# Optimization experiments

Measured on AMD Instinct MI355X. Metric: run time of the kernel, lower is better.

## Reference

```python
import jax, jax.numpy as jnp
import numpy as np

C = 512
CQ = C // 8
BN_EPS = 1e-5


def setup_inputs() -> dict:
    key = jax.random.key(0)
    ks = jax.random.split(key, 12)
    s = 0.02
    return {
        "x": jax.random.normal(ks[0], (4, C, 64, 64), dtype=jnp.float32),
        "qw": jax.random.normal(ks[1], (CQ, C), dtype=jnp.float32) * s,
        "qb": jnp.zeros((CQ,), dtype=jnp.float32),
        "kw": jax.random.normal(ks[2], (CQ, C), dtype=jnp.float32) * s,
        "kb": jnp.zeros((CQ,), dtype=jnp.float32),
        "vw": jax.random.normal(ks[3], (C, C), dtype=jnp.float32) * s,
        "vb": jnp.zeros((C,), dtype=jnp.float32),
        "gamma": jnp.zeros((1,), dtype=jnp.float32),
        "beta": jnp.zeros((1,), dtype=jnp.float32),
        "fw": jax.random.normal(ks[4], (C, 2 * C), dtype=jnp.float32) * s,
        "fb": jnp.zeros((C,), dtype=jnp.float32),
        "bn_w": jnp.ones((C,), dtype=jnp.float32),
        "bn_b": jnp.zeros((C,), dtype=jnp.float32),
    }


def reference(x, qw, qb, kw, kb, vw, vb, gamma, beta, fw, fb, bn_w, bn_b):
    b, c, h, w = x.shape
    n = h * w
    xf = x.reshape(b, c, n)  # [b, c, n]

    # ----- position attention -----
    q = jnp.einsum('oc,bcn->bon', qw, xf) + qb[None, :, None]  # [b, cq, n]
    k = jnp.einsum('oc,bcn->bon', kw, xf) + kb[None, :, None]
    v = jnp.einsum('oc,bcn->bon', vw, xf) + vb[None, :, None]  # [b, c, n]
    # scores[i, j] = q_i . k_j, softmax over j
    scores = jnp.einsum('bci,bcj->bij', q, k)  # [b, n, n]
    att = jax.nn.softmax(scores, axis=-1)
    pos = jnp.einsum('bcj,bij->bci', v, att)  # [b, c, n]
    pos_out = (gamma[0] * pos + xf).reshape(b, c, h, w)

    # ----- channel attention -----
    energy = jnp.einsum('bin,bjn->bij', xf, xf)  # [b, c, c]
    catt = jax.nn.softmax(energy, axis=-1)
    chan = jnp.einsum('bij,bjn->bin', catt, xf)
    chan_out = (beta[0] * chan + xf).reshape(b, c, h, w)

    # ----- fusion: 1x1 conv + BN (batch stats, training mode) + ReLU -----
    cat = jnp.concatenate([pos_out, chan_out], axis=1)  # [b, 2c, h, w]
    y = jnp.einsum('oc,bchw->bohw', fw, cat) + fb[None, :, None, None]
    mean = jnp.mean(y, axis=(0, 2, 3), keepdims=True)
    var = jnp.var(y, axis=(0, 2, 3), keepdims=True)
    yn = (y - mean) * jax.lax.rsqrt(var + BN_EPS)
    out = jax.nn.relu(yn * bn_w[None, :, None, None] + bn_b[None, :, None, None])
    return out
```

## Files before the change

kernel.cpp:

```cpp
#include <hip/hip_runtime.h>
#include <stdint.h>

typedef unsigned short u16;
typedef __attribute__((ext_vector_type(8))) short bf16x8;
typedef __attribute__((ext_vector_type(4))) float f32x4;

#define DEVI static __device__ __forceinline__

DEVI u16 f2bf(float f){
  union { float f; uint32_t u; } c; c.f = f;
  uint32_t u = c.u;
  u += 0x7FFFu + ((u >> 16) & 1u);
  return (u16)(u >> 16);
}
DEVI float b2f(u16 h){
  union { uint32_t u; float f; } c; c.u = ((uint32_t)h) << 16;
  return c.f;
}

DEVI void gload16(const u16* g, u16* l){
  __builtin_amdgcn_global_load_lds(
      (const __attribute__((address_space(1))) unsigned int*)g,
      (__attribute__((address_space(3))) unsigned int*)l, 16, 0, 0);
}

DEVI bf16x8 ldsrd(const void* base, int byte){
  return *reinterpret_cast<const bf16x8*>((const char*)base + byte);
}

template<int BM,int BN,int FM,int FN,int BIAS,int EPI,int SWZ,int KSPLIT=1>
__global__ __launch_bounds__(256) void gemm_bt(
    const u16* __restrict__ A, long long strideA, int lda,
    const u16* __restrict__ B, long long strideB, int ldb,
    void* __restrict__ C, long long strideC, int ldc,
    const float* __restrict__ bias, int K,
    const float* __restrict__ cscale, const u16* __restrict__ xadd,
    long long strideX, int ldx, float* __restrict__ red)
{
  constexpr int BK  = 32;
  constexpr int WTM = FM*16, WTN = FN*16;
  static_assert(BM == 2*WTM && BN == 2*WTN, "2x2 wave layout");
  __shared__ u16 As[BM*BK];
  __shared__ u16 Bs[BN*BK];

  int bx = blockIdx.x, by = blockIdx.y, bz = blockIdx.z;
  if(SWZ){
    const int gx = gridDim.x, gy = gridDim.y;
    const int nwg = gx * gy * gridDim.z;
    const int orig = bx + gx * (by + gy * bz);
    const int q = nwg >> 3, r = nwg & 7;
    const int xcd = orig & 7, i = orig >> 3;
    const int wg = (xcd < r ? xcd*(q+1) : r*(q+1) + (xcd-r)*q) + i;
    bx = wg % gx;
    const int t = wg / gx;
    by = t % gy;
    bz = t / gy;
  }

  const int zz = bz;
  const int z  = (KSPLIT > 1) ? zz / KSPLIT : zz;
  const int ks = (KSPLIT > 1) ? zz % KSPLIT : 0;
  const u16* Ab = A + (long long)z * strideA + (long long)ks * K;
  const u16* Bb = B + (long long)z * strideB + (long long)ks * K;

  const int tid  = threadIdx.x;
  const int lane = tid & 63, wid = tid >> 6;
  const int wr = wid >> 1, wc = wid & 1;
  const long long bm0 = (long long)by * BM;
  const long long bn0 = (long long)bx * BN;

  const int srow  = lane >> 2;
  const int scol  = (((lane & 3) ^ ((lane >> 3) & 3))) * 8;
  const int wrow  = wid * 16 + srow;
  constexpr int TA = BM/64, TB = BN/64;

  const int fr  = lane & 15;
  const int sl8 = ((lane >> 4) ^ ((lane >> 1) & 3)) * 8;

  f32x4 acc[FM][FN] = {};

  for(int k0 = 0; k0 < K; k0 += BK){
    __syncthreads();
    #pragma unroll
    for(int t=0;t<TA;t++)
      gload16(&Ab[(bm0 + t*64 + wrow)*lda + k0 + scol],
              &As[(t*64 + wid*16)*BK]);
    #pragma unroll
    for(int t=0;t<TB;t++)
      gload16(&Bb[(bn0 + t*64 + wrow)*ldb + k0 + scol],
              &Bs[(t*64 + wid*16)*BK]);
    __syncthreads();

    bf16x8 af[FM], bg[FN];
    #pragma unroll
    for(int m=0;m<FM;m++)
      af[m] = *reinterpret_cast<const bf16x8*>(&As[(wr*WTM + m*16 + fr)*BK + sl8]);
    #pragma unroll
    for(int n=0;n<FN;n++)
      bg[n] = *reinterpret_cast<const bf16x8*>(&Bs[(wc*WTN + n*16 + fr)*BK + sl8]);
    #pragma unroll
    for(int m=0;m<FM;m++)
      #pragma unroll
      for(int n=0;n<FN;n++)
        acc[m][n] = __builtin_amdgcn_mfma_f32_16x16x32_bf16(af[m], bg[n], acc[m][n], 0, 0, 0);
  }

  const int lr = (lane >> 4) * 4, lc = lane & 15;

  if(EPI == 8){
    u16* Cp = (u16*)C + (long long)zz*strideC;
    #pragma unroll
    for(int n=0;n<FN;n++){
      long long col = bn0 + wc*WTN + n*16 + lc;
      float bv = bias[(int)col];
      float s = 0.f, ss = 0.f;
      #pragma unroll
      for(int m=0;m<FM;m++){
        #pragma unroll
        for(int r=0;r<4;r++){
          long long row = bm0 + wr*WTM + m*16 + lr + r;
          long long idx = row*(long long)ldc + col;
          float v = acc[m][n][r] + bv + b2f(Cp[idx]);
          Cp[idx] = f2bf(v);
          s += v; ss += v*v;
        }
      }
      s += __shfl_xor(s,16); ss += __shfl_xor(ss,16);
      s += __shfl_xor(s,32); ss += __shfl_xor(ss,32);
      if(lane < 16){
        int slot = (z*(int)gridDim.y + by)*2 + wr;
        red[col*512 + slot*2]     = s;
        red[col*512 + slot*2 + 1] = ss;
      }
    }
    return;
  }

  const float g = (EPI == 3) ? cscale[0] : 0.f;
  #pragma unroll
  for(int m=0;m<FM;m++){
    #pragma unroll
    for(int n=0;n<FN;n++){
      #pragma unroll
      for(int r=0;r<4;r++){
        long long row = bm0 + wr*WTM + m*16 + lr + r;
        long long col = bn0 + wc*WTN + n*16 + lc;
        float v = acc[m][n][r];
        if(BIAS == 1) v += bias[(int)row];
        if(BIAS == 2) v += bias[(int)col];
        long long idx = row * (long long)ldc + col;
        if(EPI == 0){
          ((float*)C + (long long)zz*strideC)[idx] = v;
        } else if(EPI == 1){
          ((float*)C + (long long)zz*strideC)[idx] += v;
        } else if(EPI == 2){
          ((u16*)C + (long long)zz*strideC)[idx] = f2bf(v);
        } else {
          float xv = b2f(xadd[(long long)z*strideX + row*(long long)ldx + col]);
          ((u16*)C + (long long)zz*strideC)[idx] = f2bf(g * v + xv);
        }
      }
    }
  }
}

__global__ __launch_bounds__(512, 4) void flash_pos(
    const u16* __restrict__ qkT,
    const u16* __restrict__ vB,
    u16* __restrict__ yT,
    const float* __restrict__ gamma)
{
  __shared__ u16 Ks[2][64*64];
  __shared__ u16 Vs[256*64];
  __shared__ u16 Ps[64*64];
  __shared__ float RS[2][4][32];

  int flat = blockIdx.x + 64*(blockIdx.y + 2*blockIdx.z);
  flat = (flat & 7)*64 + (flat >> 3);
  const int bx = flat & 63;
  const int ch = (flat >> 6) & 1;
  const int z  = flat >> 7;

  const int q0 = bx*64, c0 = ch*256;
  const int tid = threadIdx.x, lane = tid & 63, wid = tid >> 6;
  const int wr = wid >> 2, wc = wid & 3;
  const int fr = lane & 15, fq = lane >> 4;

  const u16* qkb = qkT + (long long)z*4096*128;
  const u16* vbb = vB  + (long long)z*512*4096;

  const int srow  = lane >> 3;
  const int sslot = (lane & 7) ^ srow;

  bf16x8 qa[2][2];
  #pragma unroll
  for(int m=0;m<2;m++)
    #pragma unroll
    for(int kk=0;kk<2;kk++)
      qa[m][kk] = *reinterpret_cast<const bf16x8*>(
          &qkb[(long long)(q0 + wr*32 + m*16 + fr)*128 + kk*32 + fq*8]);

  const u16* kp  = qkb + (long long)(wid*8 + srow)*128 + 64 + sslot*8;
  const u16* vp0 = vbb + (long long)(c0 + wid*8 + srow)*4096 + sslot*8;

  const int xm   = (fr & 7) << 4;
  const int koff = (wc*16 + fr)*128 + ((fq*16) ^ xm);
  const int pab  = (wr*32 + fr)*128 + ((fq*16) ^ xm);
  const int vfb  = (wc*64 + fr)*128 + ((fq*16) ^ xm);
  const int kdst = wid * 1024;
  const int key2 = (wc*16 + fr)*2;
  int pwo[4];
  #pragma unroll
  for(int r=0;r<4;r++){
    int qr = fq*4 + r;
    pwo[r] = qr*128 + (key2 ^ ((qr & 7) << 4));
  }

  gload16(kp, (u16*)((char*)Ks + kdst));
  kp += 64*128;
  gload16(vp0,            &Vs[(  0 + wid*8)*64]);
  gload16(vp0 +  64*4096, &Vs[( 64 + wid*8)*64]);
  gload16(vp0 + 128*4096, &Vs[(128 + wid*8)*64]);
  gload16(vp0 + 192*4096, &Vs[(192 + wid*8)*64]);
  vp0 += 64;
  __syncthreads();

  f32x4 acc[2][4] = {};
  float rsacc[2][4] = {};

  for(int t=0;t<64;t++){
    const int kbase = (t & 1) ? 8192 : 0;
    bf16x8 kb0 = ldsrd(Ks, kbase + koff);
    bf16x8 kb1 = ldsrd(Ks, kbase + (koff ^ 64));
    f32x4 s[2] = {};
    #pragma unroll
    for(int m=0;m<2;m++){
      s[m] = __builtin_amdgcn_mfma_f32_16x16x32_bf16(qa[m][0], kb0, s[m], 0, 0, 0);
      s[m] = __builtin_amdgcn_mfma_f32_16x16x32_bf16(qa[m][1], kb1, s[m], 0, 0, 0);
    }

    #pragma unroll
    for(int m=0;m<2;m++){
      float e0 = exp2f(s[m][0]), e1 = exp2f(s[m][1]);
      float e2 = exp2f(s[m][2]), e3 = exp2f(s[m][3]);
      rsacc[m][0] += e0; rsacc[m][1] += e1;
      rsacc[m][2] += e2; rsacc[m][3] += e3;
      char* pbase = (char*)Ps + wr*4096 + m*2048;
      *(u16*)(pbase + pwo[0]) = f2bf(e0);
      *(u16*)(pbase + pwo[1]) = f2bf(e1);
      *(u16*)(pbase + pwo[2]) = f2bf(e2);
      *(u16*)(pbase + pwo[3]) = f2bf(e3);
    }
    __syncthreads();

    if(t+1 < 64){
      gload16(kp, (u16*)((char*)Ks + (kbase ^ 8192) + kdst));
      kp += 64*128;
    }

    bf16x8 pa00 = ldsrd(Ps, pab);
    bf16x8 pa01 = ldsrd(Ps, pab ^ 64);
    bf16x8 pa10 = ldsrd(Ps, (pab + 2048));
    bf16x8 pa11 = ldsrd(Ps, (pab + 2048) ^ 64);
    __builtin_amdgcn_s_setprio(1);
    #pragma unroll
    for(int n=0;n<4;n++){
      bf16x8 v0 = ldsrd(Vs, vfb + n*2048);
      bf16x8 v1 = ldsrd(Vs, (vfb + n*2048) ^ 64);
      acc[0][n] = __builtin_amdgcn_mfma_f32_16x16x32_bf16(pa00, v0, acc[0][n], 0, 0, 0);
      acc[0][n] = __builtin_amdgcn_mfma_f32_16x16x32_bf16(pa01, v1, acc[0][n], 0, 0, 0);
      acc[1][n] = __builtin_amdgcn_mfma_f32_16x16x32_bf16(pa10, v0, acc[1][n], 0, 0, 0);
      acc[1][n] = __builtin_amdgcn_mfma_f32_16x16x32_bf16(pa11, v1, acc[1][n], 0, 0, 0);
    }
    __builtin_amdgcn_s_setprio(0);
    __syncthreads();

    if(t+1 < 64){
      gload16(vp0,            &Vs[(  0 + wid*8)*64]);
      gload16(vp0 +  64*4096, &Vs[( 64 + wid*8)*64]);
      gload16(vp0 + 128*4096, &Vs[(128 + wid*8)*64]);
      gload16(vp0 + 192*4096, &Vs[(192 + wid*8)*64]);
      vp0 += 64;
    }
  }

  #pragma unroll
  for(int m=0;m<2;m++)
    #pragma unroll
    for(int r=0;r<4;r++){
      float v = rsacc[m][r];
      #pragma unroll
      for(int o=1;o<16;o<<=1) v += __shfl_xor(v, o);
      rsacc[m][r] = v;
    }
  if(fr == 0){
    #pragma unroll
    for(int m=0;m<2;m++)
      #pragma unroll
      for(int r=0;r<4;r++)
        RS[wr][wc][m*16 + fq*4 + r] = rsacc[m][r];
  }
  __syncthreads();

  const float g = gamma[0];
  u16* yb = yT + (long long)z*4096*512;
  #pragma unroll
  for(int m=0;m<2;m++){
    float inv[4];
    #pragma unroll
    for(int r=0;r<4;r++){
      int rloc = m*16 + fq*4 + r;
      inv[r] = g / (RS[wr][0][rloc] + RS[wr][1][rloc] +
                    RS[wr][2][rloc] + RS[wr][3][rloc]);
    }
    #pragma unroll
    for(int n=0;n<4;n++){
      #pragma unroll
      for(int r=0;r<4;r++){
        int qrow = q0 + wr*32 + m*16 + fq*4 + r;
        int c    = c0 + wc*64 + n*16 + fr;
        yb[(long long)qrow*512 + c] = f2bf(acc[m][n][r]*inv[r]);
      }
    }
  }
}

__global__ __launch_bounds__(256) void esum_stats(const u16* __restrict__ part,
                                                  float* __restrict__ st)
{
  const int row = blockIdx.x;
  const int b = row >> 9, i = row & 511;
  const int t = threadIdx.x;
  const int lane = t & 63, wid = t >> 6;
  float v0 = 0.f, v1 = 0.f;
  #pragma unroll
  for(int sl=0;sl<4;sl++){
    uint32_t pr = *reinterpret_cast<const uint32_t*>(
        &part[(((long long)(b*4 + sl)*512 + i)*512) + 2*t]);
    v0 += b2f((u16)pr);
    v1 += b2f((u16)(pr >> 16));
  }
  float m = fmaxf(v0, v1);
  #pragma unroll
  for(int o=32;o;o>>=1) m = fmaxf(m, __shfl_xor(m, o));
  __shared__ float sred[4];
  if(lane == 0) sred[wid] = m;
  __syncthreads();
  m = fmaxf(fmaxf(sred[0], sred[1]), fmaxf(sred[2], sred[3]));
  float s = __expf(v0 - m) + __expf(v1 - m);
  #pragma unroll
  for(int o=32;o;o>>=1) s += __shfl_xor(s, o);
  __syncthreads();
  if(lane == 0) sred[wid] = s;
  __syncthreads();
  if(t == 0){
    st[row*2]   = m;
    st[row*2+1] = sred[0] + sred[1] + sred[2] + sred[3];
  }
}

__global__ __launch_bounds__(256) void catt_apply(const u16* __restrict__ part,
                                                  const float* __restrict__ st,
                                                  u16* __restrict__ cattT)
{
  const int row = blockIdx.x;
  const int b = row >> 9, i = row & 511;
  const int t = threadIdx.x;
  float v0 = 0.f, v1 = 0.f;
  #pragma unroll
  for(int sl=0;sl<4;sl++){
    uint32_t pr = *reinterpret_cast<const uint32_t*>(
        &part[(((long long)(b*4 + sl)*512 + i)*512) + 2*t]);
    v0 += b2f((u16)pr);
    v1 += b2f((u16)(pr >> 16));
  }
  float4 ms = reinterpret_cast<const float4*>(st)[b*256 + t];
  float o0 = __expf(v0 - ms.x) / ms.y;
  float o1 = __expf(v1 - ms.z) / ms.w;
  uint32_t pk = (uint32_t)f2bf(o0) | ((uint32_t)f2bf(o1) << 16);
  *reinterpret_cast<uint32_t*>(&cattT[(long long)row * 512 + 2*t]) = pk;
}

__global__ __launch_bounds__(256) void prep_weights(
    const float* __restrict__ qw, const float* __restrict__ kw,
    const float* __restrict__ vw, const float* __restrict__ fw,
    const float* __restrict__ qb, const float* __restrict__ kb,
    u16* __restrict__ qkwb, u16* __restrict__ vwT, u16* __restrict__ fwb,
    u16* __restrict__ fw12, float* __restrict__ qkb)
{
  const float LOG2E = 1.4426950408889634f;
  long long i = (long long)blockIdx.x*256 + threadIdx.x;
  if(i < 8192){
    float4 v = reinterpret_cast<const float4*>(qw)[i];
    ushort4 w = { f2bf(v.x*LOG2E), f2bf(v.y*LOG2E), f2bf(v.z*LOG2E), f2bf(v.w*LOG2E) };
    reinterpret_cast<ushort4*>(qkwb)[i] = w;
  } else if(i < 16384){
    long long o = i - 8192;
    float4 v = reinterpret_cast<const float4*>(kw)[o];
    ushort4 w = { f2bf(v.x), f2bf(v.y), f2bf(v.z), f2bf(v.w) };
    reinterpret_cast<ushort4*>(qkwb + 32768)[o] = w;
  } else if(i < 81920){
    long long o = i - 16384;
    float4 v = reinterpret_cast<const float4*>(vw)[o];
    int c  = (int)(o >> 7);
    int cp = (int)(o & 127) * 4;
    vwT[(cp+0)*512 + c] = f2bf(v.x);
    vwT[(cp+1)*512 + c] = f2bf(v.y);
    vwT[(cp+2)*512 + c] = f2bf(v.z);
    vwT[(cp+3)*512 + c] = f2bf(v.w);
  } else if(i < 212992){
    long long o = i - 81920;
    float4 v = reinterpret_cast<const float4*>(fw)[o];
    ushort4 w = { f2bf(v.x), f2bf(v.y), f2bf(v.z), f2bf(v.w) };
    reinterpret_cast<ushort4*>(fwb)[o] = w;
    int row = (int)(o >> 8);
    int c4  = (int)(o & 255) * 4;
    if(c4 < 512){
      float4 v2 = reinterpret_cast<const float4*>(fw)[o + 128];
      ushort4 s = { f2bf(v.x+v2.x), f2bf(v.y+v2.y), f2bf(v.z+v2.z), f2bf(v.w+v2.w) };
      reinterpret_cast<ushort4*>(fw12)[row*128 + (c4>>2)] = s;
    }
  } else if(i < 213024){
    int t = (int)(i - 212992) * 4;
    #pragma unroll
    for(int j=0;j<4;j++) qkb[t+j] = (t+j < 64) ? qb[t+j]*LOG2E : kb[t+j-64];
  }
}

__global__ __launch_bounds__(256) void fwvb(const float* __restrict__ fw,
                                            const float* __restrict__ vb,
                                            float* __restrict__ bp)
{
  int o = blockIdx.x*256 + threadIdx.x;
  if(o >= 512) return;
  float s = 0.f;
  for(int c=0;c<512;c++) s += fw[o*1024 + c] * vb[c];
  bp[o] = s;
}

__global__ __launch_bounds__(256) void transpose_cast(
    const float* __restrict__ x, u16* __restrict__ xfb, u16* __restrict__ xfT)
{
  __shared__ float tile[32][33];
  const int b  = blockIdx.z;
  const int n0 = blockIdx.x * 32, c0 = blockIdx.y * 32;
  const int tx = threadIdx.x, ty = threadIdx.y;
  const float* xp = x + (long long)b * 512 * 4096;
  #pragma unroll
  for(int i=0;i<4;i++){
    int c = c0 + ty + i*8;
    float v = xp[(long long)c*4096 + n0 + tx];
    tile[ty + i*8][tx] = v;
    xfb[((long long)b*512 + c)*4096 + n0 + tx] = f2bf(v);
  }
  __syncthreads();
  #pragma unroll
  for(int i=0;i<4;i++){
    int n = n0 + ty + i*8;
    xfT[((long long)b*4096 + n)*512 + c0 + tx] = f2bf(tile[tx][ty + i*8]);
  }
}

__global__ __launch_bounds__(256) void bn_finalize(const float* __restrict__ red,
                                                   float* __restrict__ stat)
{
  int ch = blockIdx.x*256 + threadIdx.x;
  if(ch >= 512) return;
  float s = 0.f, ss = 0.f;
  for(int j=0;j<256;j++){
    s  += red[ch*512 + j*2];
    ss += red[ch*512 + j*2 + 1];
  }
  float mean = s * (1.f/16384.f);
  float var  = ss * (1.f/16384.f) - mean*mean;
  stat[ch*2]   = mean;
  stat[ch*2+1] = rsqrtf(var + 1e-5f);
}

__global__ __launch_bounds__(256) void bn_apply_t(const u16* __restrict__ yT,
    const float* __restrict__ stat, const float* __restrict__ w,
    const float* __restrict__ bb, float* __restrict__ out)
{
  __shared__ float tile[32][33];
  const int b  = blockIdx.z;
  const int n0 = blockIdx.x * 32, c0 = blockIdx.y * 32;
  const int tx = threadIdx.x, ty = threadIdx.y;
  const int ch = c0 + tx;
  const float sc = w[ch] * stat[ch*2+1];
  const float sh = bb[ch] - stat[ch*2] * sc;
  #pragma unroll
  for(int i=0;i<4;i++){
    int n = n0 + ty + i*8;
    float v = b2f(yT[((long long)b*4096 + n)*512 + ch]);
    tile[ty + i*8][tx] = fmaxf(v*sc + sh, 0.f);
  }
  __syncthreads();
  #pragma unroll
  for(int i=0;i<4;i++){
    int c = c0 + ty + i*8;
    out[((long long)b*512 + c)*4096 + n0 + tx] = tile[tx][ty + i*8];
  }
}

extern "C" void kernel_launch(void* const* d_in, const int* in_sizes, int n_in,
                              void* d_out, int out_size, void* d_ws, size_t ws_size,
                              hipStream_t stream)
{
  const float* x     = (const float*)d_in[0];
  const float* qw    = (const float*)d_in[1];
  const float* qb    = (const float*)d_in[2];
  const float* kw    = (const float*)d_in[3];
  const float* kb    = (const float*)d_in[4];
  const float* vw    = (const float*)d_in[5];
  const float* vb    = (const float*)d_in[6];
  const float* gamma = (const float*)d_in[7];
  const float* beta  = (const float*)d_in[8];
  const float* fw    = (const float*)d_in[9];
  const float* fb    = (const float*)d_in[10];
  const float* bnw   = (const float*)d_in[11];
  const float* bnb   = (const float*)d_in[12];
  float* out = (float*)d_out;
  (void)in_sizes; (void)n_in; (void)out_size; (void)ws_size;

  char* base = (char*)d_ws;
  size_t off = 0;
  auto alloc = [&](size_t bytes)->char* {
    char* p = base + off;
    off += (bytes + 255) & ~(size_t)255;
    return p;
  };
  const long long NB = 4, Cc = 512, Nn = 4096;

  u16*   xfT  = (u16*)alloc((size_t)NB*Nn*Cc*2);
  u16*   xfb  = (u16*)alloc((size_t)NB*Cc*Nn*2);
  u16*   fwb  = (u16*)alloc((size_t)Cc*2*Cc*2);
  u16*   qkwb = (u16*)alloc((size_t)128*Cc*2);
  float* qkb  = (float*)alloc(128*4);
  u16*   vwT  = (u16*)alloc((size_t)Cc*Cc*2);
  u16*   Wp   = (u16*)alloc((size_t)Cc*Cc*2);
  u16*   fw12 = (u16*)alloc((size_t)Cc*Cc*2);
  float* bp   = (float*)alloc(Cc*4);
  u16*   qkT  = (u16*)alloc((size_t)NB*Nn*128*2);
  u16*   vB   = (u16*)alloc((size_t)NB*Cc*Nn*2);
  u16*   epart= (u16*)alloc((size_t)16*Cc*Cc*2);
  u16*   cattT= (u16*)alloc((size_t)NB*Cc*Cc*2);
  u16*   Mb   = (u16*)alloc((size_t)NB*Cc*Cc*2);
  float* st2  = (float*)alloc((size_t)NB*Cc*2*4);
  float* stat = (float*)alloc((size_t)Cc*2*4);
  float* red  = (float*)alloc((size_t)Cc*256*2*4);
  u16*   yT   = xfb;

  prep_weights<<<dim3(833), dim3(256), 0, stream>>>(qw, kw, vw, fw, qb, kb,
                                                    qkwb, vwT, fwb, fw12, qkb);
  fwvb<<<dim3(2), dim3(256), 0, stream>>>(fw, vb, bp);
  transpose_cast<<<dim3(128,16,4), dim3(32,8), 0, stream>>>(x, xfb, xfT);

  gemm_bt<64,64,2,2,0,2,1><<<dim3(8,8,1), dim3(256), 0, stream>>>(
      fwb, 0, 1024, vwT, 0, 512, Wp, 0, 512, nullptr, 512,
      nullptr, nullptr, 0, 0, nullptr);

  gemm_bt<64,128,2,4,2,2,1><<<dim3(1,64,4), dim3(256), 0, stream>>>(
      xfT, Nn*Cc, 512, qkwb, 0, 512, qkT, Nn*128, 128, qkb, 512,
      nullptr, nullptr, 0, 0, nullptr);
  gemm_bt<128,128,4,4,1,2,1><<<dim3(32,4,4), dim3(256), 0, stream>>>(
      Wp, 0, 512, xfT, Nn*Cc, 512, vB, Cc*Nn, 4096, bp, 512,
      nullptr, nullptr, 0, 0, nullptr);

  gemm_bt<128,128,4,4,0,2,1,4><<<dim3(4,4,16), dim3(256), 0, stream>>>(
      xfb, Cc*Nn, 4096, xfb, Cc*Nn, 4096, epart, Cc*Cc, 512, nullptr, 1024,
      nullptr, nullptr, 0, 0, nullptr);
  esum_stats<<<dim3(2048), dim3(256), 0, stream>>>(epart, st2);
  catt_apply<<<dim3(2048), dim3(256), 0, stream>>>(epart, st2, cattT);

  gemm_bt<64,64,2,2,0,3,1><<<dim3(8,8,4), dim3(256), 0, stream>>>(
      fwb + 512, 0, 1024, cattT, Cc*Cc, 512, Mb, Cc*Cc, 512, nullptr, 512,
      beta, fw12, 0, 512, nullptr);

  flash_pos<<<dim3(64,2,4), dim3(512), 0, stream>>>(qkT, vB, yT, gamma);

  gemm_bt<128,128,4,4,2,8,1><<<dim3(4,32,4), dim3(256), 0, stream>>>(
      xfT, Nn*Cc, 512, Mb, Cc*Cc, 512, yT, Nn*Cc, 512, fb, 512,
      nullptr, nullptr, 0, 0, red);

  bn_finalize<<<dim3(2), dim3(256), 0, stream>>>(red, stat);
  bn_apply_t<<<dim3(128,16,4), dim3(32,8), 0, stream>>>(yT, stat, bnw, bnb, out);
}
```

Before: 275.8 us.

## Double flash_pos query tile to 128 rows and fold fwvb into prep_weights

The position-attention flash kernel now handles 128 queries per block instead of 64. Its 8 waves are rearranged as 4x2, so each wave computes a 32x32 score tile and a 32x128 output tile. Each K/V tile loaded into LDS is reused across twice as many queries, halving global K/V traffic and the number of blocks, at the cost of more accumulator registers (acc grows from 8 to 16 f32x4) and fewer blocks in flight (256 vs 512). The small fw·vb bias kernel is also merged into prep_weights, saving one launch.

```diff
diff --git a/kernel.cpp b/kernel.cpp
--- a/kernel.cpp
+++ b/kernel.cpp
@@ -172,18 +172,18 @@
 {
   __shared__ u16 Ks[2][64*64];
   __shared__ u16 Vs[256*64];
-  __shared__ u16 Ps[64*64];
-  __shared__ float RS[2][4][32];
-
-  int flat = blockIdx.x + 64*(blockIdx.y + 2*blockIdx.z);
-  flat = (flat & 7)*64 + (flat >> 3);
-  const int bx = flat & 63;
-  const int ch = (flat >> 6) & 1;
-  const int z  = flat >> 7;
-
-  const int q0 = bx*64, c0 = ch*256;
+  __shared__ u16 Ps[128*64];
+  __shared__ float RS[4][2][32];
+
+  int flat = blockIdx.x + 32*(blockIdx.y + 2*blockIdx.z);
+  flat = (flat & 7)*32 + (flat >> 3);
+  const int bx = flat & 31;
+  const int ch = (flat >> 5) & 1;
+  const int z  = flat >> 6;
+
+  const int q0 = bx*128, c0 = ch*256;
   const int tid = threadIdx.x, lane = tid & 63, wid = tid >> 6;
-  const int wr = wid >> 2, wc = wid & 3;
+  const int wr = wid >> 1, wc = wid & 1;
   const int fr = lane & 15, fq = lane >> 4;
 
   const u16* qkb = qkT + (long long)z*4096*128;
@@ -204,17 +204,11 @@
   const u16* vp0 = vbb + (long long)(c0 + wid*8 + srow)*4096 + sslot*8;
 
   const int xm   = (fr & 7) << 4;
-  const int koff = (wc*16 + fr)*128 + ((fq*16) ^ xm);
+  const int koff = (wc*32 + fr)*128 + ((fq*16) ^ xm);
   const int pab  = (wr*32 + fr)*128 + ((fq*16) ^ xm);
-  const int vfb  = (wc*64 + fr)*128 + ((fq*16) ^ xm);
+  const int vfb  = (wc*128 + fr)*128 + ((fq*16) ^ xm);
   const int kdst = wid * 1024;
-  const int key2 = (wc*16 + fr)*2;
-  int pwo[4];
-  #pragma unroll
-  for(int r=0;r<4;r++){
-    int qr = fq*4 + r;
-    pwo[r] = qr*128 + (key2 ^ ((qr & 7) << 4));
-  }
+  const int pkey0 = (wc*32 + fr)*2;
 
   gload16(kp, (u16*)((char*)Ks + kdst));
   kp += 64*128;
@@ -225,31 +219,40 @@
   vp0 += 64;
   __syncthreads();
 
-  f32x4 acc[2][4] = {};
+  f32x4 acc[2][8] = {};
   float rsacc[2][4] = {};
 
   for(int t=0;t<64;t++){
     const int kbase = (t & 1) ? 8192 : 0;
-    bf16x8 kb0 = ldsrd(Ks, kbase + koff);
-    bf16x8 kb1 = ldsrd(Ks, kbase + (koff ^ 64));
-    f32x4 s[2] = {};
+    bf16x8 kb[2][2];
+    #pragma unroll
+    for(int n=0;n<2;n++)
+      #pragma unroll
+      for(int kk=0;kk<2;kk++)
+        kb[n][kk] = ldsrd(Ks, kbase + ((koff + n*2048) ^ (kk*64)));
+    f32x4 s[2][2] = {};
+    #pragma unroll
+    for(int m=0;m<2;m++)
+      #pragma unroll
+      for(int n=0;n<2;n++)
+        #pragma unroll
+        for(int kk=0;kk<2;kk++)
+          s[m][n] = __builtin_amdgcn_mfma_f32_16x16x32_bf16(qa[m][kk], kb[n][kk], s[m][n], 0, 0, 0);
+
     #pragma unroll
     for(int m=0;m<2;m++){
-      s[m] = __builtin_amdgcn_mfma_f32_16x16x32_bf16(qa[m][0], kb0, s[m], 0, 0, 0);
-      s[m] = __builtin_amdgcn_mfma_f32_16x16x32_bf16(qa[m][1], kb1, s[m], 0, 0, 0);
-    }
-
-    #pragma unroll
-    for(int m=0;m<2;m++){
-      float e0 = exp2f(s[m][0]), e1 = exp2f(s[m][1]);
-      float e2 = exp2f(s[m][2]), e3 = exp2f(s[m][3]);
-      rsacc[m][0] += e0; rsacc[m][1] += e1;
-      rsacc[m][2] += e2; rsacc[m][3] += e3;
       char* pbase = (char*)Ps + wr*4096 + m*2048;
-      *(u16*)(pbase + pwo[0]) = f2bf(e0);
-      *(u16*)(pbase + pwo[1]) = f2bf(e1);
-      *(u16*)(pbase + pwo[2]) = f2bf(e2);
-      *(u16*)(pbase + pwo[3]) = f2bf(e3);
+      #pragma unroll
+      for(int n=0;n<2;n++){
+        const int pkey = pkey0 + n*32;
+        #pragma unroll
+        for(int r=0;r<4;r++){
+          float e = exp2f(s[m][n][r]);
+          rsacc[m][r] += e;
+          int qr = fq*4 + r;
+          *(u16*)(pbase + qr*128 + (pkey ^ ((qr & 7) << 4))) = f2bf(e);
+        }
+      }
     }
     __syncthreads();
 
@@ -258,19 +261,21 @@
       kp += 64*128;
     }
 
-    bf16x8 pa00 = ldsrd(Ps, pab);
-    bf16x8 pa01 = ldsrd(Ps, pab ^ 64);
-    bf16x8 pa10 = ldsrd(Ps, (pab + 2048));
-    bf16x8 pa11 = ldsrd(Ps, (pab + 2048) ^ 64);
+    bf16x8 pa[2][2];
+    #pragma unroll
+    for(int m=0;m<2;m++)
+      #pragma unroll
+      for(int kk=0;kk<2;kk++)
+        pa[m][kk] = ldsrd(Ps, (pab + m*2048) ^ (kk*64));
     __builtin_amdgcn_s_setprio(1);
     #pragma unroll
-    for(int n=0;n<4;n++){
-      bf16x8 v0 = ldsrd(Vs, vfb + n*2048);
-      bf16x8 v1 = ldsrd(Vs, (vfb + n*2048) ^ 64);
-      acc[0][n] = __builtin_amdgcn_mfma_f32_16x16x32_bf16(pa00, v0, acc[0][n], 0, 0, 0);
-      acc[0][n] = __builtin_amdgcn_mfma_f32_16x16x32_bf16(pa01, v1, acc[0][n], 0, 0, 0);
-      acc[1][n] = __builtin_amdgcn_mfma_f32_16x16x32_bf16(pa10, v0, acc[1][n], 0, 0, 0);
-      acc[1][n] = __builtin_amdgcn_mfma_f32_16x16x32_bf16(pa11, v1, acc[1][n], 0, 0, 0);
+    for(int n=0;n<8;n++){
+      #pragma unroll
+      for(int kk=0;kk<2;kk++){
+        bf16x8 v = ldsrd(Vs, (vfb + n*2048) ^ (kk*64));
+        acc[0][n] = __builtin_amdgcn_mfma_f32_16x16x32_bf16(pa[0][kk], v, acc[0][n], 0, 0, 0);
+        acc[1][n] = __builtin_amdgcn_mfma_f32_16x16x32_bf16(pa[1][kk], v, acc[1][n], 0, 0, 0);
+      }
     }
     __builtin_amdgcn_s_setprio(0);
     __syncthreads();
@@ -310,15 +315,14 @@
     #pragma unroll
     for(int r=0;r<4;r++){
       int rloc = m*16 + fq*4 + r;
-      inv[r] = g / (RS[wr][0][rloc] + RS[wr][1][rloc] +
-                    RS[wr][2][rloc] + RS[wr][3][rloc]);
-    }
-    #pragma unroll
-    for(int n=0;n<4;n++){
+      inv[r] = g / (RS[wr][0][rloc] + RS[wr][1][rloc]);
+    }
+    #pragma unroll
+    for(int n=0;n<8;n++){
       #pragma unroll
       for(int r=0;r<4;r++){
         int qrow = q0 + wr*32 + m*16 + fq*4 + r;
-        int c    = c0 + wc*64 + n*16 + fr;
+        int c    = c0 + wc*128 + n*16 + fr;
         yb[(long long)qrow*512 + c] = f2bf(acc[m][n][r]*inv[r]);
       }
     }
@@ -385,8 +389,9 @@
     const float* __restrict__ qw, const float* __restrict__ kw,
     const float* __restrict__ vw, const float* __restrict__ fw,
     const float* __restrict__ qb, const float* __restrict__ kb,
+    const float* __restrict__ vb,
     u16* __restrict__ qkwb, u16* __restrict__ vwT, u16* __restrict__ fwb,
-    u16* __restrict__ fw12, float* __restrict__ qkb)
+    u16* __restrict__ fw12, float* __restrict__ qkb, float* __restrict__ bp)
 {
   const float LOG2E = 1.4426950408889634f;
   long long i = (long long)blockIdx.x*256 + threadIdx.x;
@@ -424,18 +429,12 @@
     int t = (int)(i - 212992) * 4;
     #pragma unroll
     for(int j=0;j<4;j++) qkb[t+j] = (t+j < 64) ? qb[t+j]*LOG2E : kb[t+j-64];
-  }
-}
-
-__global__ __launch_bounds__(256) void fwvb(const float* __restrict__ fw,
-                                            const float* __restrict__ vb,
-                                            float* __restrict__ bp)
-{
-  int o = blockIdx.x*256 + threadIdx.x;
-  if(o >= 512) return;
-  float s = 0.f;
-  for(int c=0;c<512;c++) s += fw[o*1024 + c] * vb[c];
-  bp[o] = s;
+  } else if(i < 213536){
+    int o = (int)(i - 213024);
+    float s = 0.f;
+    for(int c=0;c<512;c++) s += fw[o*1024 + c] * vb[c];
+    bp[o] = s;
+  }
 }
 
 __global__ __launch_bounds__(256) void transpose_cast(
@@ -550,9 +549,8 @@
   float* red  = (float*)alloc((size_t)Cc*256*2*4);
   u16*   yT   = xfb;
 
-  prep_weights<<<dim3(833), dim3(256), 0, stream>>>(qw, kw, vw, fw, qb, kb,
-                                                    qkwb, vwT, fwb, fw12, qkb);
-  fwvb<<<dim3(2), dim3(256), 0, stream>>>(fw, vb, bp);
+  prep_weights<<<dim3(835), dim3(256), 0, stream>>>(qw, kw, vw, fw, qb, kb, vb,
+                                                    qkwb, vwT, fwb, fw12, qkb, bp);
   transpose_cast<<<dim3(128,16,4), dim3(32,8), 0, stream>>>(x, xfb, xfT);
 
   gemm_bt<64,64,2,2,0,2,1><<<dim3(8,8,1), dim3(256), 0, stream>>>(
@@ -576,7 +574,7 @@
       fwb + 512, 0, 1024, cattT, Cc*Cc, 512, Mb, Cc*Cc, 512, nullptr, 512,
       beta, fw12, 0, 512, nullptr);
 
-  flash_pos<<<dim3(64,2,4), dim3(512), 0, stream>>>(qkT, vB, yT, gamma);
+  flash_pos<<<dim3(32,2,4), dim3(512), 0, stream>>>(qkT, vB, yT, gamma);
 
   gemm_bt<128,128,4,4,2,8,1><<<dim3(4,32,4), dim3(256), 0, stream>>>(
       xfT, Nn*Cc, 512, Mb, Cc*Cc, 512, yT, Nn*Cc, 512, fb, 512,
```

After: 376.3 us. +36.4%, slower.
